# Kernel optimization log

Measured on AMD Instinct MI355X. Metric: run time of the kernel, lower is better.

The kernel has to match this reference:

```python
import jax, jax.numpy as jnp
import numpy as np

E = 8      # n_routed_experts
TOPK = 2
D = 768    # hidden_dim
F = 3072   # routed_expert_inter_dim (== shared_expert_inter_dim)


def setup_inputs() -> dict:
    key = jax.random.key(0)
    ks = jax.random.split(key, 11)
    s = 0.02
    return {
        "x": jax.random.normal(ks[0], (2, 64, 64, D), dtype=jnp.float32),
        "gate_w": jax.random.normal(ks[1], (E, D), dtype=jnp.float32),          # Gate.weight (torch randn init)
        "w1": jax.random.normal(ks[2], (E, F, D), dtype=jnp.float32) * s,       # Expert.fc1.weight per expert
        "b1": jax.random.normal(ks[3], (E, F), dtype=jnp.float32) * s,
        "w2": jax.random.normal(ks[4], (E, D, F), dtype=jnp.float32) * s,       # Expert.fc2.weight per expert
        "b2": jax.random.normal(ks[5], (E, D), dtype=jnp.float32) * s,
        "ws1": jax.random.normal(ks[6], (F, D), dtype=jnp.float32) * s,         # shared GeluMLP fc1
        "bs1": jax.random.normal(ks[7], (F,), dtype=jnp.float32) * s,
        "ws2": jax.random.normal(ks[8], (D, F), dtype=jnp.float32) * s,         # shared GeluMLP fc2
        "bs2": jax.random.normal(ks[9], (D,), dtype=jnp.float32) * s,
    }


def _gelu(v):
    return jax.nn.gelu(v, approximate=False)  # torch nn.GELU default = exact erf


def reference(x, gate_w, w1, b1, w2, b2, ws1, bs1, ws2, bs2):
    B, H, W, Dh = x.shape
    xf = x.reshape(-1, Dh)                                  # [T, D]
    T = xf.shape[0]

    # Gate: softmax over expert logits, top-k, renormalize
    scores = jax.nn.softmax(xf @ gate_w.T, axis=-1)         # [T, E]
    vals, idx = jax.lax.top_k(scores, TOPK)                 # [T, K]
    vals = vals / jnp.sum(vals, axis=-1, keepdims=True)

    # Dense combine weights: 0 for unselected experts (faithful to scatter-add)
    cw = jnp.zeros((T, E), dtype=xf.dtype).at[
        jnp.arange(T)[:, None], idx
    ].add(vals)                                             # [T, E]

    # Routed experts: small fixed structural loop over E experts
    out = jnp.zeros_like(xf)
    for e in range(E):
        h = _gelu(xf @ w1[e].T + b1[e])                     # [T, F]
        y = h @ w2[e].T + b2[e]                             # [T, D]
        out = out + y * cw[:, e:e + 1]

    # Shared expert (GeluMLP) applied to all tokens
    shared = _gelu(xf @ ws1.T + bs1) @ ws2.T + bs2          # [T, D]

    return (out + shared).reshape(B, H, W, Dh)
```

## Files before the change

kernel.cpp:

```cpp
#include <hip/hip_runtime.h>
#include <hip/hip_bf16.h>

#define T_TOK 8192
#define E_EXP 8
#define DDIM  768
#define FDIM  3072

typedef _Float16 f16x8 __attribute__((ext_vector_type(8)));
typedef _Float16 f16x4 __attribute__((ext_vector_type(4)));
typedef float    f32x4 __attribute__((ext_vector_type(4)));

static const size_t XH_OFF   = 0;
static const size_t W1H_OFF  = 12582912;
static const size_t Y_OFF    = W1H_OFF;
static const size_t W2H_OFF  = 50331648;
static const size_t WS1H_OFF = 88080384;
static const size_t WS2H_OFF = 92798976;
static const size_t H_OFF    = 97517568;
static const size_t ROWS_OFF = 198180864;
static const size_t RW_OFF   = 198246400;
static const size_t TIDX_OFF = 198311936;
static const size_t TW_OFF   = 198377472;
static const size_t CNT_OFF  = 198443008;
static const size_t BASE_OFF = 198443264;
static const size_t CUR_OFF  = 198443520;
static const size_t TSLOT_OFF= 198443776;
static const size_t WS_NEED  = 198509312;

__device__ inline float fast_gelu(float v) {
    float v2 = v * v;
    float z2n = v * __builtin_fmaf(v2, -0.0713548163f, -1.5957691216f);
    float e = __expf(z2n);
    float s = __builtin_amdgcn_rcpf(1.0f + e);
    return v * s;
}

__global__ void cvt_f32_f16(const float* __restrict__ src, _Float16* __restrict__ dst, int n4) {
    int i = blockIdx.x * blockDim.x + threadIdx.x;
    if (i >= n4) return;
    float4 v = ((const float4*)src)[i];
    f16x4 o = { (_Float16)v.x, (_Float16)v.y, (_Float16)v.z, (_Float16)v.w };
    *(f16x4*)(dst + 4 * (size_t)i) = o;
}

__global__ void gate_kernel(const float* __restrict__ x, const float* __restrict__ gw,
                            int* __restrict__ tidx, float* __restrict__ tw) {
    int wave = threadIdx.x >> 6;
    int lane = threadIdx.x & 63;
    int t = blockIdx.x * 4 + wave;
    const float4* xv = (const float4*)(x + (size_t)t * DDIM);
    float p[E_EXP];
#pragma unroll
    for (int e = 0; e < E_EXP; e++) p[e] = 0.f;
    for (int i = lane; i < DDIM / 4; i += 64) {
        float4 xv4 = xv[i];
#pragma unroll
        for (int e = 0; e < E_EXP; e++) {
            float4 g = ((const float4*)(gw + (size_t)e * DDIM))[i];
            p[e] += xv4.x * g.x + xv4.y * g.y + xv4.z * g.z + xv4.w * g.w;
        }
    }
#pragma unroll
    for (int e = 0; e < E_EXP; e++) {
#pragma unroll
        for (int off = 32; off; off >>= 1) p[e] += __shfl_xor(p[e], off);
    }
    if (lane == 0) {
        int i0 = 0;
#pragma unroll
        for (int e = 1; e < E_EXP; e++) if (p[e] > p[i0]) i0 = e;
        int i1 = (i0 == 0) ? 1 : 0;
#pragma unroll
        for (int e = 0; e < E_EXP; e++) {
            if (e == i0) continue;
            if (p[e] > p[i1]) i1 = e;
        }
        float d  = p[i1] - p[i0];
        float e1 = expf(d);
        float w0 = 1.f / (1.f + e1);
        float w1 = 1.f - w0;
        tidx[2 * t]     = i0;  tw[2 * t]     = w0;
        tidx[2 * t + 1] = i1;  tw[2 * t + 1] = w1;
    }
}

__global__ void count_kernel(const int* __restrict__ tidx, int* __restrict__ cnt,
                             int* __restrict__ base, int* __restrict__ cur) {
    int c[E_EXP];
#pragma unroll
    for (int e = 0; e < E_EXP; e++) c[e] = 0;
    for (int i = threadIdx.x; i < 2 * T_TOK; i += 1024) {
        int e = tidx[i];
#pragma unroll
        for (int k = 0; k < E_EXP; k++) c[k] += (e == k) ? 1 : 0;
    }
#pragma unroll
    for (int e = 0; e < E_EXP; e++) {
#pragma unroll
        for (int off = 32; off; off >>= 1) c[e] += __shfl_xor(c[e], off);
    }
    __shared__ int wsum[16][E_EXP];
    int lane = threadIdx.x & 63, wave = threadIdx.x >> 6;
    if (lane == 0) {
#pragma unroll
        for (int e = 0; e < E_EXP; e++) wsum[wave][e] = c[e];
    }
    __syncthreads();
    if (threadIdx.x == 0) {
        int acc = 0;
        for (int e = 0; e < E_EXP; e++) {
            int s = 0;
            for (int w = 0; w < 16; w++) s += wsum[w][e];
            cnt[e] = s; base[e] = acc; cur[e] = acc; acc += s;
        }
    }
}

__global__ void scatter_kernel(const int* __restrict__ tidx, const float* __restrict__ tw,
                               int* __restrict__ cur, int* __restrict__ rowsIdx,
                               float* __restrict__ rw, int* __restrict__ tslot) {
    int t = blockIdx.x * 256 + threadIdx.x;
    int lane = threadIdx.x & 63, wave = threadIdx.x >> 6;
    unsigned long long lt = ((unsigned long long)1 << lane) - 1ull;
    __shared__ int wcnt[8][E_EXP];
    __shared__ int wpre[8][E_EXP];
    __shared__ int bbase[E_EXP];

    int myE[2], myR[2];
#pragma unroll
    for (int k = 0; k < 2; k++) {
        int e = tidx[2 * t + k];
        myE[k] = e;
        int vw = wave * 2 + k;
        int rank = 0;
#pragma unroll
        for (int ee = 0; ee < E_EXP; ee++) {
            unsigned long long m = __ballot(e == ee);
            if (e == ee) rank = __builtin_popcountll(m & lt);
            if (lane == 0) wcnt[vw][ee] = __builtin_popcountll(m);
        }
        myR[k] = rank;
    }
    __syncthreads();
    if (threadIdx.x < E_EXP) {
        int e = threadIdx.x, acc = 0;
#pragma unroll
        for (int vw = 0; vw < 8; vw++) { wpre[vw][e] = acc; acc += wcnt[vw][e]; }
        bbase[e] = atomicAdd(&cur[e], acc);
    }
    __syncthreads();
#pragma unroll
    for (int k = 0; k < 2; k++) {
        int e = myE[k];
        int slot = bbase[e] + wpre[wave * 2 + k][e] + myR[k];
        rowsIdx[slot] = t;
        rw[slot] = tw[2 * t + k];
        tslot[2 * t + k] = slot;
    }
}

__global__ void combine_kernel(const _Float16* __restrict__ y,
                               const int* __restrict__ tslot,
                               float* __restrict__ out) {
    int idx = blockIdx.x * 256 + threadIdx.x;
    int t = idx / (DDIM / 8);
    int c = (idx % (DDIM / 8)) * 8;
    int s0 = tslot[2 * t], s1 = tslot[2 * t + 1];
    f16x8 a = *(const f16x8*)(y + (size_t)s0 * DDIM + c);
    f16x8 b = *(const f16x8*)(y + (size_t)s1 * DDIM + c);
    float4* o = (float4*)(out + (size_t)t * DDIM + c);
    float4 o0 = o[0], o1 = o[1];
    o0.x += (float)a[0] + (float)b[0];
    o0.y += (float)a[1] + (float)b[1];
    o0.z += (float)a[2] + (float)b[2];
    o0.w += (float)a[3] + (float)b[3];
    o1.x += (float)a[4] + (float)b[4];
    o1.y += (float)a[5] + (float)b[5];
    o1.z += (float)a[6] + (float)b[6];
    o1.w += (float)a[7] + (float)b[7];
    o[0] = o0; o[1] = o1;
}

#define FC1S 0
#define FC2S 1
#define FC1R 2
#define FC2R 3

#define GLL(srcp, ldsoff) __builtin_amdgcn_global_load_lds( \
    (const __attribute__((address_space(1))) void*)(srcp), \
    (__attribute__((address_space(3))) void*)(sm + (ldsoff)), 16, 0, 0)

#define STAGE_A(b, koff) do { \
    GLL(pA[0] + (koff), (b)*16384 +         wid*512); \
    GLL(pA[1] + (koff), (b)*16384 +  4096 + wid*512); \
    GLL(pA[2] + (koff), (b)*16384 +  8192 + wid*512); \
    GLL(pA[3] + (koff), (b)*16384 + 12288 + wid*512); \
} while (0)

#define STAGE_B(sl, koff) do { \
    GLL(pB[0] + (koff), 32768 + (sl)*8192 +        wid*512); \
    GLL(pB[1] + (koff), 32768 + (sl)*8192 + 4096 + wid*512); \
} while (0)

#define LDA(b) do { _Pragma("unroll") for (int i = 0; i < 4; i++) { \
    af[i][0] = *(const f16x8*)(sm + (b)*16384 + aRd + i*1024 + ch0); \
    af[i][1] = *(const f16x8*)(sm + (b)*16384 + aRd + i*1024 + ch1); } \
} while (0)

#define LDB(sl, jlo) do { \
    bf[(jlo)  ][0] = *(const f16x8*)(sm + bRd + (sl)*8192 + ((jlo)  )*1024 + ch0); \
    bf[(jlo)  ][1] = *(const f16x8*)(sm + bRd + (sl)*8192 + ((jlo)  )*1024 + ch1); \
    bf[(jlo)+1][0] = *(const f16x8*)(sm + bRd + (sl)*8192 + ((jlo)+1)*1024 + ch0); \
    bf[(jlo)+1][1] = *(const f16x8*)(sm + bRd + (sl)*8192 + ((jlo)+1)*1024 + ch1); \
} while (0)

#define MM(jlo) do { _Pragma("unroll") for (int i = 0; i < 4; i++) { \
    acc[i][(jlo)  ] = __builtin_amdgcn_mfma_f32_16x16x32_f16(af[i][0], bf[(jlo)  ][0], acc[i][(jlo)  ], 0,0,0); \
    acc[i][(jlo)+1] = __builtin_amdgcn_mfma_f32_16x16x32_f16(af[i][0], bf[(jlo)+1][0], acc[i][(jlo)+1], 0,0,0); \
    acc[i][(jlo)  ] = __builtin_amdgcn_mfma_f32_16x16x32_f16(af[i][1], bf[(jlo)  ][1], acc[i][(jlo)  ], 0,0,0); \
    acc[i][(jlo)+1] = __builtin_amdgcn_mfma_f32_16x16x32_f16(af[i][1], bf[(jlo)+1][1], acc[i][(jlo)+1], 0,0,0); } \
} while (0)

#define BARRIER __builtin_amdgcn_s_barrier()
#define PRIO1 __builtin_amdgcn_s_setprio(1)
#define PRIO0 __builtin_amdgcn_s_setprio(0)
#define VM6 asm volatile("s_waitcnt vmcnt(6)" ::: "memory")

template <int MODE>
__global__ __launch_bounds__(512, 2) void gemm_kernel(
    const _Float16* __restrict__ Abase,
    const _Float16* __restrict__ Wbase,
    const float* __restrict__ biasBase,
    _Float16* __restrict__ h,
    float* __restrict__ out,
    const int* __restrict__ cnt, const int* __restrict__ base,
    const int* __restrict__ rowsIdx, const float* __restrict__ rw)
{
    constexpr int K = (MODE == FC1S || MODE == FC1R) ? DDIM : FDIM;
    constexpr int N = (MODE == FC1S || MODE == FC1R) ? FDIM : DDIM;
    constexpr bool ROUTED = (MODE == FC1R || MODE == FC2R);
    constexpr int NI2 = K / 256;

    int m0, mEnd;
    const _Float16* W;
    const float* bias;
    if constexpr (ROUTED) {
        int bx = blockIdx.x, accb = 0, expert = -1, rb = 0;
#pragma unroll
        for (int e = 0; e < E_EXP; e++) {
            int nb = (cnt[e] + 255) >> 8;
            if (expert < 0 && bx < accb + nb) { expert = e; rb = bx - accb; }
            accb += nb;
        }
        if (expert < 0) return;
        m0   = base[expert] + rb * 256;
        mEnd = base[expert] + cnt[expert];
        W    = Wbase + (size_t)expert * N * K;
        bias = biasBase + (size_t)expert * N;
    } else {
        m0 = blockIdx.x * 256;
        mEnd = T_TOK;
        W = Wbase;
        bias = biasBase;
    }
    int n0 = blockIdx.y * 128;

    __shared__ __align__(16) _Float16 sm[65536];

    int tid  = threadIdx.x;
    int lane = tid & 63;
    int wid  = tid >> 6;
    int wm   = wid >> 1;
    int wn   = wid & 1;
    int m16  = lane & 15, q = lane >> 4;
    int x7   = m16 & 7;

    f32x4 acc[4][4];
#pragma unroll
    for (int i = 0; i < 4; i++)
#pragma unroll
        for (int j = 0; j < 4; j++) acc[i][j] = f32x4{0.f, 0.f, 0.f, 0.f};

    int r0  = tid >> 3;
    int cSw = (tid & 7) ^ (r0 & 7);
    const _Float16* pA[4];
    const _Float16* pB[2];
#pragma unroll
    for (int j = 0; j < 4; j++) {
        int tr = (j >> 1) * 128 + (j & 1) * 64 + r0;
        int pr = m0 + tr;
        bool valid = pr < mEnd;
        int ar;
        if constexpr (MODE == FC1R) ar = rowsIdx[valid ? pr : m0];
        else                        ar = valid ? pr : m0;
        pA[j] = Abase + (size_t)ar * K + cSw * 8;
    }
#pragma unroll
    for (int s = 0; s < 2; s++)
        pB[s] = W + (size_t)(n0 + s * 64 + r0) * K + cSw * 8;

    int aRd = (wm >> 1) * 8192 + ((wm & 1) * 64 + m16) * 64;
    int bRd = 32768 + (wn * 64 + m16) * 64;
    int ch0 = (q ^ x7) * 8;
    int ch1 = ((4 + q) ^ x7) * 8;

    f16x8 af[4][2], bf[4][2];

    STAGE_A(0, 0);
    STAGE_B(0, 0);
    STAGE_A(1, 64);
    STAGE_B(1, 64);
#pragma unroll
    for (int j = 0; j < 4; j++) pA[j] += 128;
#pragma unroll
    for (int s = 0; s < 2; s++) pB[s] += 128;
    asm volatile("s_waitcnt vmcnt(6)" ::: "memory");
    BARRIER;

#pragma unroll 1
    for (int tt = 0; tt < NI2; ++tt) {
        LDA(0); LDB(0, 0); STAGE_B(2, 0);
        BARRIER; PRIO1; MM(0); PRIO0; BARRIER;

        LDB(0, 2); STAGE_A(0, 0);
        BARRIER; PRIO1; MM(2); PRIO0; VM6; BARRIER;

        LDA(1); LDB(1, 0); STAGE_B(3, 64);
        BARRIER; PRIO1; MM(0); PRIO0; BARRIER;

        LDB(1, 2); STAGE_A(1, 64);
        BARRIER; PRIO1; MM(2); PRIO0; VM6; BARRIER;

        LDA(0); LDB(2, 0); STAGE_B(0, 128);
        BARRIER; PRIO1; MM(0); PRIO0; BARRIER;

        LDB(2, 2); STAGE_A(0, 128);
        BARRIER; PRIO1; MM(2); PRIO0; VM6; BARRIER;

        LDA(1); LDB(3, 0); STAGE_B(1, 192);
        BARRIER; PRIO1; MM(0); PRIO0; BARRIER;

        LDB(3, 2); STAGE_A(1, 192);
        BARRIER; PRIO1; MM(2); PRIO0; VM6; BARRIER;

#pragma unroll
        for (int j = 0; j < 4; j++) pA[j] += 256;
#pragma unroll
        for (int s = 0; s < 2; s++) pB[s] += 256;
    }

    asm volatile("s_waitcnt vmcnt(0)" ::: "memory");

    float biasv[4];
#pragma unroll
    for (int j = 0; j < 4; j++) biasv[j] = bias[n0 + wn * 64 + j * 16 + m16];

#pragma unroll
    for (int i = 0; i < 4; i++) {
#pragma unroll
        for (int r = 0; r < 4; r++) {
            int rowp = m0 + wm * 64 + i * 16 + q * 4 + r;
            if (rowp >= mEnd) continue;
            float wgt = 0.f;
            if constexpr (MODE == FC2R) wgt = rw[rowp];
#pragma unroll
            for (int j = 0; j < 4; j++) {
                int col = n0 + wn * 64 + j * 16 + m16;
                float v = acc[i][j][r] + biasv[j];
                if constexpr (MODE == FC1S || MODE == FC1R) {
                    v = fast_gelu(v);
                    h[(size_t)rowp * FDIM + col] = (_Float16)v;
                } else if constexpr (MODE == FC2S) {
                    out[(size_t)rowp * DDIM + col] = v;
                } else {
                    h[(size_t)rowp * DDIM + col] = (_Float16)(v * wgt);
                }
            }
        }
    }
}

#undef GLL
#undef STAGE_A
#undef STAGE_B
#undef LDA
#undef LDB
#undef MM
#undef BARRIER
#undef PRIO1
#undef PRIO0
#undef VM6

extern "C" void kernel_launch(void* const* d_in, const int* in_sizes, int n_in,
                              void* d_out, int out_size, void* d_ws, size_t ws_size,
                              hipStream_t stream) {
    const float* x   = (const float*)d_in[0];
    const float* gw  = (const float*)d_in[1];
    const float* w1  = (const float*)d_in[2];
    const float* b1  = (const float*)d_in[3];
    const float* w2  = (const float*)d_in[4];
    const float* b2  = (const float*)d_in[5];
    const float* ws1 = (const float*)d_in[6];
    const float* bs1 = (const float*)d_in[7];
    const float* ws2 = (const float*)d_in[8];
    const float* bs2 = (const float*)d_in[9];
    float* out = (float*)d_out;
    char* ws = (char*)d_ws;
    if (ws_size < WS_NEED) return;

    _Float16* xh   = (_Float16*)(ws + XH_OFF);
    _Float16* w1h  = (_Float16*)(ws + W1H_OFF);
    _Float16* yb   = (_Float16*)(ws + Y_OFF);
    _Float16* w2h  = (_Float16*)(ws + W2H_OFF);
    _Float16* ws1h = (_Float16*)(ws + WS1H_OFF);
    _Float16* ws2h = (_Float16*)(ws + WS2H_OFF);
    _Float16* h    = (_Float16*)(ws + H_OFF);
    int*   rowsIdx = (int*)(ws + ROWS_OFF);
    float* rw      = (float*)(ws + RW_OFF);
    int*   tidx    = (int*)(ws + TIDX_OFF);
    float* tw      = (float*)(ws + TW_OFF);
    int*   cnt     = (int*)(ws + CNT_OFF);
    int*   base    = (int*)(ws + BASE_OFF);
    int*   cur     = (int*)(ws + CUR_OFF);
    int*   tslot   = (int*)(ws + TSLOT_OFF);

    cvt_f32_f16<<<6144,  256, 0, stream>>>(x,   xh,   1572864);
    cvt_f32_f16<<<18432, 256, 0, stream>>>(w1,  w1h,  4718592);
    cvt_f32_f16<<<18432, 256, 0, stream>>>(w2,  w2h,  4718592);
    cvt_f32_f16<<<2304,  256, 0, stream>>>(ws1, ws1h, 589824);
    cvt_f32_f16<<<2304,  256, 0, stream>>>(ws2, ws2h, 589824);

    gate_kernel<<<2048, 256, 0, stream>>>(x, gw, tidx, tw);
    count_kernel<<<1, 1024, 0, stream>>>(tidx, cnt, base, cur);
    scatter_kernel<<<32, 256, 0, stream>>>(tidx, tw, cur, rowsIdx, rw, tslot);

    gemm_kernel<FC1S><<<dim3(32, 24), 512, 0, stream>>>(xh, ws1h, bs1, h, out, cnt, base, rowsIdx, rw);
    gemm_kernel<FC2S><<<dim3(32, 6),  512, 0, stream>>>(h,  ws2h, bs2, h, out, cnt, base, rowsIdx, rw);
    gemm_kernel<FC1R><<<dim3(72, 24), 512, 0, stream>>>(xh, w1h,  b1,  h, out, cnt, base, rowsIdx, rw);
    gemm_kernel<FC2R><<<dim3(72, 6),  512, 0, stream>>>(h,  w2h,  b2,  yb, out, cnt, base, rowsIdx, rw);

    combine_kernel<<<3072, 256, 0, stream>>>(yb, tslot, out);
}
```

Baseline: 611.0 us.

## Replace split-phase GEMM pipeline with 3-stage LDS ring buffer, one barrier per tile

Restructures the GEMM main loop from a double-buffered A / 4-slot B scheme with two barriers per half-tile into a 3-slot ring of 64-wide K tiles. Each tile prefetches the tile two steps ahead, loads all A/B fragments at once, issues 32 MFMAs, and then waits and synchronizes with a single barrier. The aim is to cut barrier count and improve overlap between global-to-LDS loads and MFMA work. In exchange, LDS use grows from 128KB to 144KB per block and fragment registers rise. With launch bounds of 2 blocks per CU, this may reduce occupancy if 2x144KB exceeds the LDS capacity.

```diff
diff --git a/kernel.cpp b/kernel.cpp
--- a/kernel.cpp
+++ b/kernel.cpp
@@ -186,45 +186,56 @@
 #define FC1R 2
 #define FC2R 3
 
-#define GLL(srcp, ldsoff) __builtin_amdgcn_global_load_lds( \
-    (const __attribute__((address_space(1))) void*)(srcp), \
-    (__attribute__((address_space(3))) void*)(sm + (ldsoff)), 16, 0, 0)
-
-#define STAGE_A(b, koff) do { \
-    GLL(pA[0] + (koff), (b)*16384 +         wid*512); \
-    GLL(pA[1] + (koff), (b)*16384 +  4096 + wid*512); \
-    GLL(pA[2] + (koff), (b)*16384 +  8192 + wid*512); \
-    GLL(pA[3] + (koff), (b)*16384 + 12288 + wid*512); \
-} while (0)
-
-#define STAGE_B(sl, koff) do { \
-    GLL(pB[0] + (koff), 32768 + (sl)*8192 +        wid*512); \
-    GLL(pB[1] + (koff), 32768 + (sl)*8192 + 4096 + wid*512); \
-} while (0)
-
-#define LDA(b) do { _Pragma("unroll") for (int i = 0; i < 4; i++) { \
-    af[i][0] = *(const f16x8*)(sm + (b)*16384 + aRd + i*1024 + ch0); \
-    af[i][1] = *(const f16x8*)(sm + (b)*16384 + aRd + i*1024 + ch1); } \
-} while (0)
-
-#define LDB(sl, jlo) do { \
-    bf[(jlo)  ][0] = *(const f16x8*)(sm + bRd + (sl)*8192 + ((jlo)  )*1024 + ch0); \
-    bf[(jlo)  ][1] = *(const f16x8*)(sm + bRd + (sl)*8192 + ((jlo)  )*1024 + ch1); \
-    bf[(jlo)+1][0] = *(const f16x8*)(sm + bRd + (sl)*8192 + ((jlo)+1)*1024 + ch0); \
-    bf[(jlo)+1][1] = *(const f16x8*)(sm + bRd + (sl)*8192 + ((jlo)+1)*1024 + ch1); \
-} while (0)
-
-#define MM(jlo) do { _Pragma("unroll") for (int i = 0; i < 4; i++) { \
-    acc[i][(jlo)  ] = __builtin_amdgcn_mfma_f32_16x16x32_f16(af[i][0], bf[(jlo)  ][0], acc[i][(jlo)  ], 0,0,0); \
-    acc[i][(jlo)+1] = __builtin_amdgcn_mfma_f32_16x16x32_f16(af[i][0], bf[(jlo)+1][0], acc[i][(jlo)+1], 0,0,0); \
-    acc[i][(jlo)  ] = __builtin_amdgcn_mfma_f32_16x16x32_f16(af[i][1], bf[(jlo)  ][1], acc[i][(jlo)  ], 0,0,0); \
-    acc[i][(jlo)+1] = __builtin_amdgcn_mfma_f32_16x16x32_f16(af[i][1], bf[(jlo)+1][1], acc[i][(jlo)+1], 0,0,0); } \
-} while (0)
-
+#define GLL(p, off16) __builtin_amdgcn_global_load_lds( \
+    (const __attribute__((address_space(1))) void*)(p), \
+    (__attribute__((address_space(3))) void*)(sm + (off16)), 16, 0, 0)
 #define BARRIER __builtin_amdgcn_s_barrier()
 #define PRIO1 __builtin_amdgcn_s_setprio(1)
 #define PRIO0 __builtin_amdgcn_s_setprio(0)
 #define VM6 asm volatile("s_waitcnt vmcnt(6)" ::: "memory")
+#define VM0 asm volatile("s_waitcnt vmcnt(0)" ::: "memory")
+
+#define TILE(S, T) do { \
+    if ((T) + 2 < NT) { \
+        constexpr int S2 = ((S) + 2) % 3; \
+        GLL(pA[0] + 128, S2 * 16384 +         wid * 512); \
+        GLL(pA[1] + 128, S2 * 16384 +  4096 + wid * 512); \
+        GLL(pA[2] + 128, S2 * 16384 +  8192 + wid * 512); \
+        GLL(pA[3] + 128, S2 * 16384 + 12288 + wid * 512); \
+        GLL(pB[0] + 128, 49152 + S2 * 8192 +        wid * 512); \
+        GLL(pB[1] + 128, 49152 + S2 * 8192 + 4096 + wid * 512); \
+    } \
+    { \
+        f16x8 af0[4], af1[4], bf0[4], bf1[4]; \
+        _Pragma("unroll") \
+        for (int i = 0; i < 4; i++) { \
+            af0[i] = *(const f16x8*)(sm + (S) * 16384 + aRd + i * 1024 + ch0); \
+            af1[i] = *(const f16x8*)(sm + (S) * 16384 + aRd + i * 1024 + ch1); \
+        } \
+        _Pragma("unroll") \
+        for (int j = 0; j < 4; j++) { \
+            bf0[j] = *(const f16x8*)(sm + 49152 + (S) * 8192 + bRd + j * 1024 + ch0); \
+            bf1[j] = *(const f16x8*)(sm + 49152 + (S) * 8192 + bRd + j * 1024 + ch1); \
+        } \
+        PRIO1; \
+        _Pragma("unroll") \
+        for (int i = 0; i < 4; i++) \
+            _Pragma("unroll") \
+            for (int j = 0; j < 4; j++) \
+                acc[i][j] = __builtin_amdgcn_mfma_f32_16x16x32_f16(af0[i], bf0[j], acc[i][j], 0, 0, 0); \
+        _Pragma("unroll") \
+        for (int i = 0; i < 4; i++) \
+            _Pragma("unroll") \
+            for (int j = 0; j < 4; j++) \
+                acc[i][j] = __builtin_amdgcn_mfma_f32_16x16x32_f16(af1[i], bf1[j], acc[i][j], 0, 0, 0); \
+        PRIO0; \
+    } \
+    if ((T) < NT - 2) { VM6; } else if ((T) == NT - 2) { VM0; } \
+    BARRIER; \
+    _Pragma("unroll") \
+    for (int g = 0; g < 4; g++) pA[g] += 64; \
+    pB[0] += 64; pB[1] += 64; \
+} while (0)
 
 template <int MODE>
 __global__ __launch_bounds__(512, 2) void gemm_kernel(
@@ -239,7 +250,8 @@
     constexpr int K = (MODE == FC1S || MODE == FC1R) ? DDIM : FDIM;
     constexpr int N = (MODE == FC1S || MODE == FC1R) ? FDIM : DDIM;
     constexpr bool ROUTED = (MODE == FC1R || MODE == FC2R);
-    constexpr int NI2 = K / 256;
+    constexpr int NT = K / 64;
+    static_assert(NT % 3 == 0, "ring unroll needs NT % 3 == 0");
 
     int m0, mEnd;
     const _Float16* W;
@@ -265,7 +277,7 @@
     }
     int n0 = blockIdx.y * 128;
 
-    __shared__ __align__(16) _Float16 sm[65536];
+    __shared__ __align__(16) _Float16 sm[73728];
 
     int tid  = threadIdx.x;
     int lane = tid & 63;
@@ -283,73 +295,46 @@
 
     int r0  = tid >> 3;
     int cSw = (tid & 7) ^ (r0 & 7);
-    const _Float16* pA[4];
-    const _Float16* pB[2];
-#pragma unroll
-    for (int j = 0; j < 4; j++) {
-        int tr = (j >> 1) * 128 + (j & 1) * 64 + r0;
-        int pr = m0 + tr;
+    const _Float16 *pA[4], *pB[2];
+#pragma unroll
+    for (int g = 0; g < 4; g++) {
+        int pr = m0 + g * 64 + r0;
         bool valid = pr < mEnd;
         int ar;
         if constexpr (MODE == FC1R) ar = rowsIdx[valid ? pr : m0];
         else                        ar = valid ? pr : m0;
-        pA[j] = Abase + (size_t)ar * K + cSw * 8;
-    }
-#pragma unroll
-    for (int s = 0; s < 2; s++)
-        pB[s] = W + (size_t)(n0 + s * 64 + r0) * K + cSw * 8;
-
-    int aRd = (wm >> 1) * 8192 + ((wm & 1) * 64 + m16) * 64;
-    int bRd = 32768 + (wn * 64 + m16) * 64;
+        pA[g] = Abase + (size_t)ar * K + cSw * 8;
+    }
+#pragma unroll
+    for (int g = 0; g < 2; g++)
+        pB[g] = W + (size_t)(n0 + g * 64 + r0) * K + cSw * 8;
+
+    int aRd = (wm * 64 + m16) * 64;
+    int bRd = (wn * 64 + m16) * 64;
     int ch0 = (q ^ x7) * 8;
     int ch1 = ((4 + q) ^ x7) * 8;
 
-    f16x8 af[4][2], bf[4][2];
-
-    STAGE_A(0, 0);
-    STAGE_B(0, 0);
-    STAGE_A(1, 64);
-    STAGE_B(1, 64);
-#pragma unroll
-    for (int j = 0; j < 4; j++) pA[j] += 128;
-#pragma unroll
-    for (int s = 0; s < 2; s++) pB[s] += 128;
-    asm volatile("s_waitcnt vmcnt(6)" ::: "memory");
+    GLL(pA[0], 0 +         wid * 512);
+    GLL(pA[1], 0 +  4096 + wid * 512);
+    GLL(pA[2], 0 +  8192 + wid * 512);
+    GLL(pA[3], 0 + 12288 + wid * 512);
+    GLL(pB[0], 49152 +        wid * 512);
+    GLL(pB[1], 49152 + 4096 + wid * 512);
+    GLL(pA[0] + 64, 16384 +         wid * 512);
+    GLL(pA[1] + 64, 16384 +  4096 + wid * 512);
+    GLL(pA[2] + 64, 16384 +  8192 + wid * 512);
+    GLL(pA[3] + 64, 16384 + 12288 + wid * 512);
+    GLL(pB[0] + 64, 49152 + 8192 +        wid * 512);
+    GLL(pB[1] + 64, 49152 + 8192 + 4096 + wid * 512);
+    VM6;
     BARRIER;
 
-#pragma unroll 1
-    for (int tt = 0; tt < NI2; ++tt) {
-        LDA(0); LDB(0, 0); STAGE_B(2, 0);
-        BARRIER; PRIO1; MM(0); PRIO0; BARRIER;
-
-        LDB(0, 2); STAGE_A(0, 0);
-        BARRIER; PRIO1; MM(2); PRIO0; VM6; BARRIER;
-
-        LDA(1); LDB(1, 0); STAGE_B(3, 64);
-        BARRIER; PRIO1; MM(0); PRIO0; BARRIER;
-
-        LDB(1, 2); STAGE_A(1, 64);
-        BARRIER; PRIO1; MM(2); PRIO0; VM6; BARRIER;
-
-        LDA(0); LDB(2, 0); STAGE_B(0, 128);
-        BARRIER; PRIO1; MM(0); PRIO0; BARRIER;
-
-        LDB(2, 2); STAGE_A(0, 128);
-        BARRIER; PRIO1; MM(2); PRIO0; VM6; BARRIER;
-
-        LDA(1); LDB(3, 0); STAGE_B(1, 192);
-        BARRIER; PRIO1; MM(0); PRIO0; BARRIER;
-
-        LDB(3, 2); STAGE_A(1, 192);
-        BARRIER; PRIO1; MM(2); PRIO0; VM6; BARRIER;
-
-#pragma unroll
-        for (int j = 0; j < 4; j++) pA[j] += 256;
-#pragma unroll
-        for (int s = 0; s < 2; s++) pB[s] += 256;
-    }
-
-    asm volatile("s_waitcnt vmcnt(0)" ::: "memory");
+    for (int t3 = 0; t3 < NT; t3 += 3) {
+        TILE(0, t3 + 0);
+        TILE(1, t3 + 1);
+        TILE(2, t3 + 2);
+    }
+    VM0;
 
     float biasv[4];
 #pragma unroll
@@ -381,15 +366,12 @@
 }
 
 #undef GLL
-#undef STAGE_A
-#undef STAGE_B
-#undef LDA
-#undef LDB
-#undef MM
 #undef BARRIER
 #undef PRIO1
 #undef PRIO0
 #undef VM6
+#undef VM0
+#undef TILE
 
 extern "C" void kernel_launch(void* const* d_in, const int* in_sizes, int n_in,
                               void* d_out, int out_size, void* d_ws, size_t ws_size,
```

After: 593.1 us. 2.9% less time.
